# Optimization experiments

Measured on AMD Instinct MI355X. Metric: run time of the kernel, lower is better.

Reference implementation:

```python
import jax, jax.numpy as jnp
import numpy as np

B, N, DIM = 8, 8192, 512
H, DH = 8, 64
INNER = H * DH
EPS = 1e-5


def setup_inputs() -> dict:
    key = jax.random.key(0)
    ks = jax.random.split(key, 5)
    x = jax.random.normal(ks[0], (B, N, DIM), dtype=jnp.float32)
    w_qkv = jax.random.normal(ks[1], (DIM, 3 * INNER), dtype=jnp.float32) * (DIM ** -0.5)
    ln_w = jnp.ones((INNER,), dtype=jnp.float32)
    ln_b = jnp.zeros((INNER,), dtype=jnp.float32)
    w_out = jax.random.normal(ks[2], (INNER, DIM), dtype=jnp.float32) * (INNER ** -0.5)
    b_out = jnp.zeros((DIM,), dtype=jnp.float32)
    return {"x": x, "w_qkv": w_qkv, "ln_w": ln_w, "ln_b": ln_b,
            "w_out": w_out, "b_out": b_out}


def _layernorm(x, w, b):
    mu = jnp.mean(x, axis=-1, keepdims=True)
    var = jnp.mean(jnp.square(x - mu), axis=-1, keepdims=True)
    return (x - mu) * jax.lax.rsqrt(var + EPS) * w + b


def reference(x, w_qkv, ln_w, ln_b, w_out, b_out):
    b, n, _ = x.shape
    qkv = x @ w_qkv  # [b, n, 3*inner]
    q, k, v = jnp.split(qkv, 3, axis=-1)
    # b n (h d) -> b h n d
    def heads(t):
        return t.reshape(b, n, H, DH).transpose(0, 2, 1, 3)
    q, k, v = heads(q), heads(k), heads(v)
    q = jax.nn.relu(q)
    k = jax.nn.relu(k)
    kv = jnp.einsum('bhnm,bhnd->bhmd', k, v)   # [b, h, d, d]
    out = jnp.einsum('bhnm,bhmd->bhnd', q, kv)  # [b, h, n, d]
    out = out.transpose(0, 2, 1, 3).reshape(b, n, INNER)
    out = _layernorm(out, ln_w, ln_b)
    return out @ w_out + b_out
```

## Files before the change

kernel.cpp:

```cpp
#include <hip/hip_runtime.h>
#include <stdint.h>

#define B_ 8
#define N_ 8192
#define DIM_ 512
#define H_ 8
#define DH_ 64
#define ROWS (B_*N_)
#define TRIPLE (3*DIM_)
#define EPS_ 1e-5f
#define PLANE ((size_t)ROWS * 64)

typedef __attribute__((ext_vector_type(8))) short short8;
typedef __attribute__((ext_vector_type(4))) float f32x4;
typedef __attribute__((ext_vector_type(4))) float fl4;
typedef __attribute__((ext_vector_type(4))) unsigned short us4;
typedef __attribute__((ext_vector_type(8))) unsigned short us8;

#define AS1 __attribute__((address_space(1)))
#define AS3 __attribute__((address_space(3)))

__device__ __forceinline__ void gld16(const void* g, void* l) {
    __builtin_amdgcn_global_load_lds((const AS1 void*)(uintptr_t)g,
                                     (AS3 void*)(unsigned)(uintptr_t)l, 16, 0, 0);
}

__device__ inline unsigned short f2bf(float f) {
    union { float f; unsigned int u; } x; x.f = f;
    unsigned int r = x.u + 0x7fffu + ((x.u >> 16) & 1u);
    return (unsigned short)(r >> 16);
}
__device__ inline float bf2f(unsigned short b) {
    union { unsigned int u; float f; } x; x.u = ((unsigned int)b) << 16;
    return x.f;
}

__device__ __forceinline__ int eoff(int row, int col) {
    return row * 64 + (col ^ ((((unsigned)row >> 2) & 3) << 4));
}

__device__ __forceinline__ int aoff(int row, int col) {
    return row * 512 + ((((col >> 3) ^ (row & 7)) << 3) | (col & 7));
}

__global__ __launch_bounds__(256) void k_cvt(const float* __restrict__ x,
                                             unsigned short* __restrict__ xb) {
    size_t i = ((size_t)blockIdx.x * 256 + threadIdx.x) * 8;
    fl4 a = *(const fl4*)(x + i);
    fl4 b = *(const fl4*)(x + i + 4);
    us8 r;
    r[0] = f2bf(a[0]); r[1] = f2bf(a[1]); r[2] = f2bf(a[2]); r[3] = f2bf(a[3]);
    r[4] = f2bf(b[0]); r[5] = f2bf(b[1]); r[6] = f2bf(b[2]); r[7] = f2bf(b[3]);
    *(us8*)(xb + i) = r;
}

__global__ __launch_bounds__(256) void k_prep(const float* __restrict__ wq,
        const float* __restrict__ wo,
        unsigned short* __restrict__ wqT, unsigned short* __restrict__ woT) {
    __shared__ float T[32][33];
    int bid = blockIdx.x;
    const float* src; unsigned short* dst; int srcCols, dstCols, k0, n0;
    if (bid < 768) {
        int tn = bid % 48, tk = bid / 48;
        src = wq; dst = wqT; srcCols = 1536; dstCols = 512;
        k0 = tk * 32; n0 = tn * 32;
    } else {
        int b = bid - 768;
        int tn = b % 16, tk = b / 16;
        src = wo; dst = woT; srcCols = 512; dstCols = 512;
        k0 = tk * 32; n0 = tn * 32;
    }
    int t = threadIdx.x, r = t >> 3, c4 = (t & 7) * 4;
    fl4 v = *(const fl4*)(src + (size_t)(k0 + r) * srcCols + n0 + c4);
    T[c4 + 0][r] = v[0]; T[c4 + 1][r] = v[1];
    T[c4 + 2][r] = v[2]; T[c4 + 3][r] = v[3];
    __syncthreads();
    us4 o;
    o[0] = f2bf(T[r][c4 + 0]); o[1] = f2bf(T[r][c4 + 1]);
    o[2] = f2bf(T[r][c4 + 2]); o[3] = f2bf(T[r][c4 + 3]);
    *(us4*)(dst + (size_t)(n0 + r) * dstCols + k0 + c4) = o;
}

__global__ __launch_bounds__(512, 4) void k_qkv8(const unsigned short* __restrict__ xb,
        const unsigned short* __restrict__ wT,
        unsigned short* __restrict__ qkv)
{
    __shared__ __align__(1024) unsigned short LDSb[3][12288];

    const int tid  = threadIdx.x;
    const int lane = tid & 63;
    const int wid  = tid >> 6;
    const int wr   = wid >> 1;
    const int wc   = wid & 1;
    const int lr   = lane & 15;

    int id  = blockIdx.x;
    int nid = (id & 7) * 384 + (id >> 3);
    int n0  = (nid % 12) * 128;
    int m0  = (nid / 12) * 256;

    const unsigned short* pA[2];
    const unsigned short* pB1;
    unsigned ldstA[2], ldstB;
#pragma unroll
    for (int j = 0; j < 2; ++j) {
        int s    = tid + j * 512;
        int row  = ((s >> 6) << 4) + ((s >> 2) & 15);
        int colb = ((s & 3) << 4) ^ (((s >> 5) & 1) << 5);
        pA[j] = xb + (size_t)(m0 + row) * 512 + (colb >> 1);
        ldstA[j] = (unsigned)((j * 512 + wid * 64) * 8);
    }
    {
        int s    = tid;
        int row  = ((s >> 6) << 4) + ((s >> 2) & 15);
        int colb = ((s & 3) << 4) ^ (((s >> 5) & 1) << 5);
        pB1 = wT + (size_t)(n0 + row) * 512 + (colb >> 1);
        ldstB = (unsigned)(8192 + wid * 64 * 8);
    }
    const int kg = (lane >> 4) * 8;
    const int lo = lr * 32 + (kg ^ ((lr >> 3) << 4));

    auto STAGE = [&](int t, int slot) {
        gld16(pA[0] + t * 32, (void*)&LDSb[slot][ldstA[0]]);
        gld16(pA[1] + t * 32, (void*)&LDSb[slot][ldstA[1]]);
        gld16(pB1   + t * 32, (void*)&LDSb[slot][ldstB]);
    };

    f32x4 acc[4][4] = {};
    short8 af[4], bfr[4];

    STAGE(0, 0);
    STAGE(1, 1);

#define WAITV(n) asm volatile("s_waitcnt vmcnt(" #n ")" ::: "memory")
#pragma unroll
    for (int t = 0; t < 16; ++t) {
        if (t <= 14) WAITV(3);
        else         WAITV(0);
        __builtin_amdgcn_s_barrier();
        __builtin_amdgcn_sched_barrier(0);

        if (t + 2 < 16) STAGE(t + 2, (t + 2) % 3);

        const unsigned short* L = LDSb[t % 3];
#pragma unroll
        for (int m = 0; m < 4; ++m)
            af[m] = *(const short8*)&L[(wr * 4 + m) * 512 + lo];
#pragma unroll
        for (int n = 0; n < 4; ++n)
            bfr[n] = *(const short8*)&L[8192 + (wc * 4 + n) * 512 + lo];

        __builtin_amdgcn_s_setprio(1);
#pragma unroll
        for (int m = 0; m < 4; ++m)
#pragma unroll
            for (int n = 0; n < 4; ++n)
                acc[m][n] = __builtin_amdgcn_mfma_f32_16x16x32_bf16(af[m], bfr[n], acc[m][n], 0, 0, 0);
        __builtin_amdgcn_s_setprio(0);
    }
#undef WAITV

    __syncthreads();

    unsigned short* S = ((unsigned short*)LDSb) + wid * 4096;
    const bool relu_tile = (n0 < 1024);
#pragma unroll
    for (int m = 0; m < 4; ++m) {
        int rbase = m * 16 + ((lane >> 4) << 2);
#pragma unroll
        for (int n = 0; n < 4; ++n) {
            int col = n * 16 + lr;
#pragma unroll
            for (int r = 0; r < 4; ++r) {
                float v = acc[m][n][r];
                if (relu_tile && v < 0.0f) v = 0.0f;
                S[eoff(rbase + r, col)] = f2bf(v);
            }
        }
    }
    __syncthreads();
    {
        int rsub = lane >> 3, sub = lane & 7;
        size_t grow = (size_t)(m0 + wr * 64);
        unsigned short* pb = qkv + (size_t)((n0 >> 6) + wc) * PLANE;
#pragma unroll
        for (int rd = 0; rd < 8; ++rd) {
            int row = rd * 8 + rsub;
            short8 vv = *(const short8*)&S[eoff(row, sub * 8)];
            *(short8*)(pb + (grow + row) * 64 + sub * 8) = vv;
        }
    }
}

__global__ __launch_bounds__(256) void k_qkv_f(const float* __restrict__ x,
        const unsigned short* __restrict__ wT,
        unsigned short* __restrict__ qkv)
{
    __shared__ unsigned short As[128][40];
    __shared__ unsigned short Bs[128][40];
    int t = threadIdx.x;
    int lane = t & 63, wave = t >> 6;
    int m0 = blockIdx.y * 128;
    int n0 = blockIdx.x * 128;
    int wm = (wave & 1) * 64, wn = (wave >> 1) * 64;
    int lr = lane & 15, kg = (lane >> 4) * 8;

    f32x4 acc[4][4] = {};
    for (int k0 = 0; k0 < DIM_; k0 += 32) {
#pragma unroll
        for (int i = 0; i < 4; ++i) {
            int c = t + 256 * i;
            int r = c >> 3, c4 = (c & 7) * 4;
            fl4 v = *(const fl4*)(x + (size_t)(m0 + r) * DIM_ + k0 + c4);
            unsigned short* dst = &As[r][c4];
            dst[0] = f2bf(v[0]); dst[1] = f2bf(v[1]); dst[2] = f2bf(v[2]); dst[3] = f2bf(v[3]);
        }
#pragma unroll
        for (int i = 0; i < 2; ++i) {
            int c = t + 256 * i;
            int r = c >> 2, c8 = (c & 3) * 8;
            *(int4*)&Bs[r][c8] = *(const int4*)(wT + (size_t)(n0 + r) * DIM_ + k0 + c8);
        }
        __syncthreads();
        short8 af[4], bfr[4];
#pragma unroll
        for (int i = 0; i < 4; ++i) af[i]  = *(short8*)&As[wm + i*16 + lr][kg];
#pragma unroll
        for (int j = 0; j < 4; ++j) bfr[j] = *(short8*)&Bs[wn + j*16 + lr][kg];
#pragma unroll
        for (int i = 0; i < 4; ++i)
#pragma unroll
            for (int j = 0; j < 4; ++j)
                acc[i][j] = __builtin_amdgcn_mfma_f32_16x16x32_bf16(af[i], bfr[j], acc[i][j], 0, 0, 0);
        __syncthreads();
    }
#pragma unroll
    for (int i = 0; i < 4; ++i) {
        int row = m0 + wm + i*16 + (lane >> 4) * 4;
#pragma unroll
        for (int j = 0; j < 4; ++j) {
            int col = n0 + wn + j*16 + (lane & 15);
            bool rl = (col < 1024);
            size_t pbase = (size_t)(col >> 6) * PLANE + (col & 63);
#pragma unroll
            for (int r = 0; r < 4; ++r) {
                float v = acc[i][j][r];
                if (rl && v < 0.0f) v = 0.0f;
                qkv[pbase + (size_t)(row + r) * 64] = f2bf(v);
            }
        }
    }
}

__global__ __launch_bounds__(256) void k_kv(const unsigned short* __restrict__ qkv,
                                            float* __restrict__ kv)
{
    __shared__ unsigned short KT[64][136];
    __shared__ unsigned short VT[64][136];
    __shared__ float red[64 * 64];
    int t = threadIdx.x, lane = t & 63, wave = t >> 6;
    int bh = blockIdx.x;
    int b = bh >> 3, h = bh & 7;
    int chunk = blockIdx.y;
    size_t rowbase = (size_t)b * N_ + (size_t)chunk * 1024;
    const unsigned short* kp = qkv + (size_t)(8 + h) * PLANE;
    const unsigned short* vp = qkv + (size_t)(16 + h) * PLANE;
    int lr = lane & 15;

    f32x4 acc[4][4] = {};
    for (int tile = 0; tile < 8; ++tile) {
        size_t r0 = rowbase + tile * 128;
#pragma unroll
        for (int i = 0; i < 2; ++i) {
            int u = t + 256 * i;
            int rp = u >> 3;
            int c8 = (u & 7) * 8;
            size_t ra = r0 + 2 * rp, rb = ra + 1;
            us8 ka = *(const us8*)(kp + ra * 64 + c8);
            us8 kb = *(const us8*)(kp + rb * 64 + c8);
            us8 va = *(const us8*)(vp + ra * 64 + c8);
            us8 vb = *(const us8*)(vp + rb * 64 + c8);
#pragma unroll
            for (int j = 0; j < 8; ++j) {
                int d = c8 + j;
                *(unsigned int*)&KT[d][2 * rp] =
                    (unsigned int)ka[j] | ((unsigned int)kb[j] << 16);
                *(unsigned int*)&VT[d][2 * rp] =
                    (unsigned int)va[j] | ((unsigned int)vb[j] << 16);
            }
        }
        __syncthreads();
        int kg = wave * 32 + (lane >> 4) * 8;
        short8 af[4], bfr[4];
#pragma unroll
        for (int i = 0; i < 4; ++i) af[i]  = *(short8*)&KT[i*16 + lr][kg];
#pragma unroll
        for (int j = 0; j < 4; ++j) bfr[j] = *(short8*)&VT[j*16 + lr][kg];
#pragma unroll
        for (int i = 0; i < 4; ++i)
#pragma unroll
            for (int j = 0; j < 4; ++j)
                acc[i][j] = __builtin_amdgcn_mfma_f32_16x16x32_bf16(af[i], bfr[j], acc[i][j], 0, 0, 0);
        __syncthreads();
    }
    for (int w = 0; w < 4; ++w) {
        if (wave == w) {
#pragma unroll
            for (int i = 0; i < 4; ++i)
#pragma unroll
                for (int j = 0; j < 4; ++j)
#pragma unroll
                    for (int r = 0; r < 4; ++r) {
                        int m = i*16 + (lane >> 4) * 4 + r;
                        int d = j*16 + (lane & 15);
                        if (w == 0) red[m * 64 + d] = acc[i][j][r];
                        else        red[m * 64 + d] += acc[i][j][r];
                    }
        }
        __syncthreads();
    }
    float* kvout = kv + (size_t)bh * 4096;
#pragma unroll
    for (int i = 0; i < 16; ++i) {
        int idx = t + 256 * i;
        atomicAdd(&kvout[idx], red[idx]);
    }
}

__global__ __launch_bounds__(256) void k_kvt(const float* __restrict__ kv,
                                             unsigned short* __restrict__ kvtb) {
    __shared__ float T[64][65];
    int bh = blockIdx.x, t = threadIdx.x;
    const float* src = kv + (size_t)bh * 4096;
    unsigned short* dst = kvtb + (size_t)bh * 4096;
#pragma unroll
    for (int i = 0; i < 16; ++i) {
        int idx = t + 256 * i;
        T[idx & 63][idx >> 6] = src[idx];
    }
    __syncthreads();
#pragma unroll
    for (int i = 0; i < 16; ++i) {
        int idx = t + 256 * i;
        dst[idx] = f2bf(T[idx >> 6][idx & 63]);
    }
}

__global__ __launch_bounds__(512, 2) void k_ao(
        const unsigned short* __restrict__ qkv,
        const unsigned short* __restrict__ kvtb,
        const float* __restrict__ lnw, const float* __restrict__ lnb,
        const unsigned short* __restrict__ woutT,
        const float* __restrict__ bout, float* __restrict__ out)
{
    __shared__ unsigned short attnS[128 * 512];
    __shared__ float lwS[512], lbS[512], muS[128], rsS[128];
    int t = threadIdx.x, lane = t & 63, wave = t >> 6;
    int lr = lane & 15;
    size_t r0 = (size_t)blockIdx.x * 128;
    int b = (int)(r0 / N_);

    for (int i = t; i < 512; i += 512) { lwS[i] = lnw[i]; lbS[i] = lnb[i]; }

    float s4[4] = {}, ss4[4] = {};

#pragma unroll
    for (int h = 0; h < H_; ++h) {
        const unsigned short* qp  = qkv + (size_t)h * PLANE;
        const unsigned short* kvh = kvtb + (size_t)(b * 8 + h) * 4096;
        f32x4 acc[4] = {};
#pragma unroll
        for (int ks = 0; ks < 2; ++ks) {
            int kg = ks * 32 + (lane >> 4) * 8;
            short8 af, bfr[4];
            af = *(const short8*)(qp + (r0 + wave * 16 + lr) * 64 + kg);
#pragma unroll
            for (int j = 0; j < 4; ++j)
                bfr[j] = *(const short8*)(kvh + (j * 16 + lr) * 64 + kg);
#pragma unroll
            for (int j = 0; j < 4; ++j)
                acc[j] = __builtin_amdgcn_mfma_f32_16x16x32_bf16(af, bfr[j], acc[j], 0, 0, 0);
        }
        int rbase = wave * 16 + (lane >> 4) * 4;
#pragma unroll
        for (int j = 0; j < 4; ++j) {
            int col = h * 64 + j * 16 + lr;
#pragma unroll
            for (int r = 0; r < 4; ++r) {
                float v = acc[j][r];
                s4[r] += v;
                ss4[r] += v * v;
                attnS[aoff(rbase + r, col)] = f2bf(v);
            }
        }
    }

#pragma unroll
    for (int q = 0; q < 4; ++q) {
        float s = s4[q], ss = ss4[q];
        s += __shfl_xor(s, 1);  ss += __shfl_xor(ss, 1);
        s += __shfl_xor(s, 2);  ss += __shfl_xor(ss, 2);
        s += __shfl_xor(s, 4);  ss += __shfl_xor(ss, 4);
        s += __shfl_xor(s, 8);  ss += __shfl_xor(ss, 8);
        s4[q] = s; ss4[q] = ss;
    }
    if (lr == 0) {
#pragma unroll
        for (int q = 0; q < 4; ++q) {
            int row = wave * 16 + (lane >> 4) * 4 + q;
            float m = s4[q] * (1.0f / 512.0f);
            muS[row] = m;
            rsS[row] = rsqrtf(ss4[q] * (1.0f / 512.0f) - m * m + EPS_);
        }
    }
    __syncthreads();

    {
        int row = t >> 2, ch = (t & 3) * 16;
        float mm = muS[row], rr = rsS[row];
        unsigned short* base = attnS + row * 512;
#pragma unroll
        for (int g = 0; g < 16; ++g) {
            int colg = ch + g;
            us8* p = (us8*)(base + ((colg ^ (row & 7)) << 3));
            us8 v = *p, o;
#pragma unroll
            for (int j = 0; j < 8; ++j)
                o[j] = f2bf((bf2f(v[j]) - mm) * rr * lwS[colg * 8 + j] + lbS[colg * 8 + j]);
            *p = o;
        }
    }
    __syncthreads();

    {
        int ncol = wave * 64;
        f32x4 acc[8][4] = {};
        for (int k0 = 0; k0 < 512; k0 += 32) {
            int gk = (k0 >> 3) + (lane >> 4);
            short8 af[8], bfr[4];
#pragma unroll
            for (int m = 0; m < 8; ++m) {
                int row = m * 16 + lr;
                af[m] = *(const short8*)&attnS[row * 512 + ((gk ^ (row & 7)) << 3)];
            }
#pragma unroll
            for (int j = 0; j < 4; ++j)
                bfr[j] = *(const short8*)(woutT + (size_t)(ncol + j * 16 + lr) * 512 + k0 + (lane >> 4) * 8);
#pragma unroll
            for (int m = 0; m < 8; ++m)
#pragma unroll
                for (int j = 0; j < 4; ++j)
                    acc[m][j] = __builtin_amdgcn_mfma_f32_16x16x32_bf16(af[m], bfr[j], acc[m][j], 0, 0, 0);
        }
#pragma unroll
        for (int m = 0; m < 8; ++m) {
            size_t row = r0 + m * 16 + ((lane >> 4) << 2);
#pragma unroll
            for (int j = 0; j < 4; ++j) {
                int col = ncol + j * 16 + (lane & 15);
                float bo = bout[col];
#pragma unroll
                for (int r = 0; r < 4; ++r)
                    out[(row + r) * DIM_ + col] = acc[m][j][r] + bo;
            }
        }
    }
}

extern "C" void kernel_launch(void* const* d_in, const int* in_sizes, int n_in,
                              void* d_out, int out_size, void* d_ws, size_t ws_size,
                              hipStream_t stream) {
    (void)in_sizes; (void)n_in; (void)out_size;
    const float* x     = (const float*)d_in[0];
    const float* w_qkv = (const float*)d_in[1];
    const float* ln_w  = (const float*)d_in[2];
    const float* ln_b  = (const float*)d_in[3];
    const float* w_out = (const float*)d_in[4];
    const float* b_out = (const float*)d_in[5];
    float* out = (float*)d_out;

    char* ws = (char*)d_ws;
    const size_t QKV_BYTES = (size_t)ROWS * TRIPLE * sizeof(unsigned short);
    const size_t KV_BYTES  = (size_t)64 * 64 * 64 * sizeof(float);
    const size_t WQT_BYTES = (size_t)TRIPLE * DIM_ * sizeof(unsigned short);
    const size_t WOT_BYTES = (size_t)DIM_ * DIM_ * sizeof(unsigned short);
    const size_t KVT_BYTES = (size_t)64 * 64 * 64 * sizeof(unsigned short);
    const size_t XB_BYTES  = (size_t)ROWS * DIM_ * sizeof(unsigned short);
    unsigned short* qkv   = (unsigned short*)ws;
    float*          kvbuf = (float*)(ws + QKV_BYTES);
    unsigned short* wqkvT = (unsigned short*)(ws + QKV_BYTES + KV_BYTES);
    unsigned short* woutT = (unsigned short*)(ws + QKV_BYTES + KV_BYTES + WQT_BYTES);
    unsigned short* kvtb  = (unsigned short*)(ws + QKV_BYTES + KV_BYTES + WQT_BYTES + WOT_BYTES);
    unsigned short* xb    = (unsigned short*)(ws + QKV_BYTES + KV_BYTES + WQT_BYTES + WOT_BYTES + KVT_BYTES);
    const size_t NEED = QKV_BYTES + KV_BYTES + WQT_BYTES + WOT_BYTES + KVT_BYTES + XB_BYTES;

    hipMemsetAsync(kvbuf, 0, KV_BYTES, stream);
    k_prep<<<1024, 256, 0, stream>>>(w_qkv, w_out, wqkvT, woutT);
    if (ws_size >= NEED) {
        k_cvt<<<16384, 256, 0, stream>>>(x, xb);
        k_qkv8<<<dim3(3072), 512, 0, stream>>>(xb, wqkvT, qkv);
    } else {
        k_qkv_f<<<dim3(12, 512), 256, 0, stream>>>(x, wqkvT, qkv);
    }
    k_kv<<<dim3(64, 8), 256, 0, stream>>>(qkv, kvbuf);
    k_kvt<<<64, 256, 0, stream>>>(kvbuf, kvtb);
    k_ao<<<512, 512, 0, stream>>>(qkv, kvtb, ln_w, ln_b, woutT, b_out, out);
}
```

Baseline: 496.4 us.

## Fuse fp32-to-bf16 conversion of x into QKV GEMM A-tile staging

Removes the separate k_cvt kernel and its bf16 copy of x. The QKV GEMM now loads fp32 x into registers, converts to bf16 and writes it into LDS itself, while the weights still arrive by direct global-to-LDS loads. This saves the 128MB write and read of xb plus one kernel launch. In exchange each of the 12 column-tile blocks rereads the A rows in fp32 (twice the bytes), the pipeline needs more registers, and an extra barrier is added per k-step.

```diff
diff --git a/kernel.cpp b/kernel.cpp
--- a/kernel.cpp
+++ b/kernel.cpp
@@ -41,17 +41,6 @@
 
 __device__ __forceinline__ int aoff(int row, int col) {
     return row * 512 + ((((col >> 3) ^ (row & 7)) << 3) | (col & 7));
-}
-
-__global__ __launch_bounds__(256) void k_cvt(const float* __restrict__ x,
-                                             unsigned short* __restrict__ xb) {
-    size_t i = ((size_t)blockIdx.x * 256 + threadIdx.x) * 8;
-    fl4 a = *(const fl4*)(x + i);
-    fl4 b = *(const fl4*)(x + i + 4);
-    us8 r;
-    r[0] = f2bf(a[0]); r[1] = f2bf(a[1]); r[2] = f2bf(a[2]); r[3] = f2bf(a[3]);
-    r[4] = f2bf(b[0]); r[5] = f2bf(b[1]); r[6] = f2bf(b[2]); r[7] = f2bf(b[3]);
-    *(us8*)(xb + i) = r;
 }
 
 __global__ __launch_bounds__(256) void k_prep(const float* __restrict__ wq,
@@ -81,7 +70,7 @@
     *(us4*)(dst + (size_t)(n0 + r) * dstCols + k0 + c4) = o;
 }
 
-__global__ __launch_bounds__(512, 4) void k_qkv8(const unsigned short* __restrict__ xb,
+__global__ __launch_bounds__(512, 4) void k_qkv8(const float* __restrict__ x,
         const unsigned short* __restrict__ wT,
         unsigned short* __restrict__ qkv)
 {
@@ -99,17 +88,18 @@
     int n0  = (nid % 12) * 128;
     int m0  = (nid / 12) * 256;
 
-    const unsigned short* pA[2];
-    const unsigned short* pB1;
-    unsigned ldstA[2], ldstB;
+    const float* pAx[2];
+    unsigned ldstA[2];
 #pragma unroll
     for (int j = 0; j < 2; ++j) {
         int s    = tid + j * 512;
         int row  = ((s >> 6) << 4) + ((s >> 2) & 15);
         int colb = ((s & 3) << 4) ^ (((s >> 5) & 1) << 5);
-        pA[j] = xb + (size_t)(m0 + row) * 512 + (colb >> 1);
-        ldstA[j] = (unsigned)((j * 512 + wid * 64) * 8);
-    }
+        pAx[j] = x + (size_t)(m0 + row) * 512 + (colb >> 1);
+        ldstA[j] = (unsigned)(s * 8);
+    }
+    const unsigned short* pB1;
+    unsigned ldstB;
     {
         int s    = tid;
         int row  = ((s >> 6) << 4) + ((s >> 2) & 15);
@@ -120,27 +110,46 @@
     const int kg = (lane >> 4) * 8;
     const int lo = lr * 32 + (kg ^ ((lr >> 3) << 4));
 
-    auto STAGE = [&](int t, int slot) {
-        gld16(pA[0] + t * 32, (void*)&LDSb[slot][ldstA[0]]);
-        gld16(pA[1] + t * 32, (void*)&LDSb[slot][ldstA[1]]);
-        gld16(pB1   + t * 32, (void*)&LDSb[slot][ldstB]);
+    fl4 aS[2][4];
+
+    auto ISSUE = [&](int t, int p) {
+        gld16(pB1 + t * 32, (void*)&LDSb[t % 3][ldstB]);
+#pragma unroll
+        for (int j = 0; j < 2; ++j) {
+            aS[p][2*j]   = *(const fl4*)(pAx[j] + t * 32);
+            aS[p][2*j+1] = *(const fl4*)(pAx[j] + t * 32 + 4);
+        }
+    };
+    auto CVTWRITE = [&](int t, int p) {
+#pragma unroll
+        for (int j = 0; j < 2; ++j) {
+            us8 o;
+#pragma unroll
+            for (int e = 0; e < 4; ++e) {
+                o[e]     = f2bf(aS[p][2*j][e]);
+                o[4 + e] = f2bf(aS[p][2*j+1][e]);
+            }
+            *(us8*)&LDSb[t % 3][ldstA[j]] = o;
+        }
     };
 
     f32x4 acc[4][4] = {};
     short8 af[4], bfr[4];
 
-    STAGE(0, 0);
-    STAGE(1, 1);
-
 #define WAITV(n) asm volatile("s_waitcnt vmcnt(" #n ")" ::: "memory")
+#define LGKM0    asm volatile("s_waitcnt lgkmcnt(0)" ::: "memory")
+
+    ISSUE(0, 0);
+    ISSUE(1, 1);
+    WAITV(5);
+    CVTWRITE(0, 0);
+    LGKM0;
+    __builtin_amdgcn_s_barrier();
+    __builtin_amdgcn_sched_barrier(0);
+
 #pragma unroll
     for (int t = 0; t < 16; ++t) {
-        if (t <= 14) WAITV(3);
-        else         WAITV(0);
-        __builtin_amdgcn_s_barrier();
-        __builtin_amdgcn_sched_barrier(0);
-
-        if (t + 2 < 16) STAGE(t + 2, (t + 2) % 3);
+        if (t + 2 < 16) ISSUE(t + 2, t & 1);
 
         const unsigned short* L = LDSb[t % 3];
 #pragma unroll
@@ -157,8 +166,17 @@
             for (int n = 0; n < 4; ++n)
                 acc[m][n] = __builtin_amdgcn_mfma_f32_16x16x32_bf16(af[m], bfr[n], acc[m][n], 0, 0, 0);
         __builtin_amdgcn_s_setprio(0);
+
+        if (t + 1 < 16) {
+            if (t + 2 < 16) WAITV(5); else WAITV(0);
+            CVTWRITE(t + 1, (t + 1) & 1);
+            LGKM0;
+            __builtin_amdgcn_s_barrier();
+            __builtin_amdgcn_sched_barrier(0);
+        }
     }
 #undef WAITV
+#undef LGKM0
 
     __syncthreads();
 
@@ -485,20 +503,17 @@
     const size_t WQT_BYTES = (size_t)TRIPLE * DIM_ * sizeof(unsigned short);
     const size_t WOT_BYTES = (size_t)DIM_ * DIM_ * sizeof(unsigned short);
     const size_t KVT_BYTES = (size_t)64 * 64 * 64 * sizeof(unsigned short);
-    const size_t XB_BYTES  = (size_t)ROWS * DIM_ * sizeof(unsigned short);
     unsigned short* qkv   = (unsigned short*)ws;
     float*          kvbuf = (float*)(ws + QKV_BYTES);
     unsigned short* wqkvT = (unsigned short*)(ws + QKV_BYTES + KV_BYTES);
     unsigned short* woutT = (unsigned short*)(ws + QKV_BYTES + KV_BYTES + WQT_BYTES);
     unsigned short* kvtb  = (unsigned short*)(ws + QKV_BYTES + KV_BYTES + WQT_BYTES + WOT_BYTES);
-    unsigned short* xb    = (unsigned short*)(ws + QKV_BYTES + KV_BYTES + WQT_BYTES + WOT_BYTES + KVT_BYTES);
-    const size_t NEED = QKV_BYTES + KV_BYTES + WQT_BYTES + WOT_BYTES + KVT_BYTES + XB_BYTES;
+    const size_t NEED = QKV_BYTES + KV_BYTES + WQT_BYTES + WOT_BYTES + KVT_BYTES;
 
     hipMemsetAsync(kvbuf, 0, KV_BYTES, stream);
     k_prep<<<1024, 256, 0, stream>>>(w_qkv, w_out, wqkvT, woutT);
     if (ws_size >= NEED) {
-        k_cvt<<<16384, 256, 0, stream>>>(x, xb);
-        k_qkv8<<<dim3(3072), 512, 0, stream>>>(xb, wqkvT, qkv);
+        k_qkv8<<<dim3(3072), 512, 0, stream>>>(x, wqkvT, qkv);
     } else {
         k_qkv_f<<<dim3(12, 512), 256, 0, stream>>>(x, wqkvT, qkv);
     }
```

New measurement: 950.5 us. 1.91x slower.
